# Optimization experiments

Measured on AMD Instinct MI355X. Metric: run time of the kernel, lower is better.

## Reference

```python
import jax, jax.numpy as jnp
import numpy as np

D = 30  # input/hidden size
H1 = 15  # head hidden size


def _rnn_layer(x, Wih, Whh, bih, bhh):
    # x: [B,T,D]; vanilla tanh RNN, h_t = tanh(x_t Wih^T + b_ih + h_{t-1} Whh^T + b_hh)
    xw = jnp.einsum('btd,hd->bth', x, Wih) + bih + bhh  # precompute input projection
    h0 = jnp.zeros((x.shape[0], Whh.shape[0]), x.dtype)

    def step(h, xt):
        h = jnp.tanh(xt + h @ Whh.T)
        return h, h

    _, ys = jax.lax.scan(step, h0, jnp.swapaxes(xw, 0, 1))  # scan over time
    return jnp.swapaxes(ys, 0, 1)  # [B,T,H]


def setup_inputs() -> dict:
    key = jax.random.key(0)
    ks = jax.random.split(key, 16)
    s = 1.0 / np.sqrt(D)
    u = lambda k, shape, sc: jax.random.uniform(k, shape, jnp.float32, -sc, sc)
    return {
        'x': jax.random.normal(ks[0], (4096, 512, D), jnp.float32),
        'Wih1': u(ks[1], (D, D), s), 'Whh1': u(ks[2], (D, D), s),
        'bih1': u(ks[3], (D,), s), 'bhh1': u(ks[4], (D,), s),
        'Wih2': u(ks[5], (D, D), s), 'Whh2': u(ks[6], (D, D), s),
        'bih2': u(ks[7], (D,), s), 'bhh2': u(ks[8], (D,), s),
        'W1': u(ks[9], (H1, D), s), 'b1': u(ks[10], (H1,), s),
        'W2': u(ks[11], (H1, H1), 1.0 / np.sqrt(H1)), 'b2': u(ks[12], (H1,), 1.0 / np.sqrt(H1)),
        'W3': u(ks[13], (1, H1), 1.0 / np.sqrt(H1)), 'b3': u(ks[14], (1,), 1.0 / np.sqrt(H1)),
    }


def reference(x, Wih1, Whh1, bih1, bhh1, Wih2, Whh2, bih2, bhh2, W1, b1, W2, b2, W3, b3):
    out = _rnn_layer(x, Wih1, Whh1, bih1, bhh1)
    # Dropout(0.23) is identity in eval mode
    out = _rnn_layer(out, Wih2, Whh2, bih2, bhh2)
    out = jnp.tanh(out @ W1.T + b1)
    out = jnp.tanh(out @ W2.T + b2)
    return out @ W3.T + b3  # [B,T,1]
```

## Files before the change

### kernel.cpp

```cpp
#include <hip/hip_runtime.h>


namespace {
constexpr int T = 512;
constexpr int D = 30;
constexpr int H = 15;

__device__ __forceinline__ float fast_tanh(float x) {
  float e = __expf(2.0f * x);
  return 1.0f - 2.0f * __builtin_amdgcn_rcpf(e + 1.0f);
}

__device__ __forceinline__ float bcast(float v, int lane) {
  return __int_as_float(__builtin_amdgcn_readlane(__float_as_int(v), lane));
}

__device__ __forceinline__ float lanepull(float v, int byteaddr) {
  return __int_as_float(
      __builtin_amdgcn_ds_bpermute(byteaddr, __float_as_int(v)));
}

#define PIN(v) asm("" : "+v"(v))
}

__global__ __launch_bounds__(256) void xw_precompute(
    const float* __restrict__ x, const float* __restrict__ Wih1,
    const float* __restrict__ bih1, const float* __restrict__ bhh1,
    float* __restrict__ xw) {
  __shared__ float xs[256 * 31];
  const int tid = threadIdx.x;
  const long base = (long)blockIdx.x * (256 * 30);

#pragma unroll
  for (int k = 0; k < 15; ++k) {
    const int idx = k * 512 + tid * 2;
    const float2 v = *(const float2*)(x + base + idx);
    const int row = idx / 30;
    const int col = idx - row * 30;
    xs[row * 31 + col] = v.x;
    xs[row * 31 + col + 1] = v.y;
  }
  __syncthreads();

  float xv[D];
#pragma unroll
  for (int k = 0; k < D; ++k) xv[k] = xs[tid * 31 + k];
#pragma unroll
  for (int i = 0; i < D; ++i) {
    float a = bih1[i] + bhh1[i];
#pragma unroll
    for (int k = 0; k < D; ++k) a = fmaf(Wih1[i * D + k], xv[k], a);
    xs[tid * 31 + i] = a;
  }
  __syncthreads();

#pragma unroll
  for (int k = 0; k < 15; ++k) {
    const int idx = k * 512 + tid * 2;
    const int row = idx / 30;
    const int col = idx - row * 30;
    float2 o;
    o.x = xs[row * 31 + col];
    o.y = xs[row * 31 + col + 1];
    *(float2*)(xw + base + idx) = o;
  }
}

__global__ __attribute__((amdgpu_waves_per_eu(4, 4)))
__launch_bounds__(64) void rnn_head_rec(
    const float* __restrict__ xw,
    const float* __restrict__ Whh1,
    const float* __restrict__ Wih2, const float* __restrict__ Whh2,
    const float* __restrict__ bih2, const float* __restrict__ bhh2,
    const float* __restrict__ W1, const float* __restrict__ b1,
    const float* __restrict__ W2, const float* __restrict__ b2,
    const float* __restrict__ W3, const float* __restrict__ b3,
    float* __restrict__ out) {
  const int j = threadIdx.x;
  const bool lo = (j < 32);
  const int ju = j & 31;
  const int r = (ju < D) ? ju : (D - 1);

  float aw[D], bw[D];
  {
    const float* Ar = (lo ? Whh1 : Wih2) + r * D;
#pragma unroll
    for (int k = 0; k < D; ++k) aw[k] = Ar[k];
#pragma unroll
    for (int k = 0; k < D; ++k) {
      float v;
      if (!lo)
        v = Whh2[r * D + k];
      else if (j < H)
        v = W1[j * D + k];
      else if (j >= 16 && j < 31 && k < H)
        v = W2[(j - 16) * H + k];
      else
        v = 0.0f;
      bw[k] = v;
    }
  }
#pragma unroll
  for (int k = 0; k < D; ++k) {
    PIN(aw[k]);
    PIN(bw[k]);
  }

  int addr2[H];
  {
    const int abase = (j >= 16 && j < 32) ? 0 : 128;
#pragma unroll
    for (int k = 0; k < H; ++k) {
      addr2[k] = abase + 4 * k;
      PIN(addr2[k]);
    }
  }

  float biasA2m = lo ? 0.0f : (bih2[r] + bhh2[r]);
  float biasB = (j < H) ? b1[j] : ((j >= 16 && j < 31) ? b2[j - 16] : 0.0f);
  const bool mid = (j >= 16) && (j < 31);
  float w3v = mid ? W3[j - 16] : 0.0f;
  const float sb3 = b3[0];
  PIN(biasA2m);
  PIN(biasB);
  PIN(w3v);

  const float* xr = xw + (long)blockIdx.x * (T * D);
  float* outp = out + (long)blockIdx.x * T;
  const int cj = r;

  float xvA = xr[cj];
  float xvB = xr[D + cj];

  float rec1 = 0.0f;
  float rec2 = 0.0f;
  float v1p = 0.0f;

  auto step = [&](float& xv, int tpre) -> float {
    const float h1 = fast_tanh(xv + rec1);

    xv = xr[(long)tpre * D + cj];

    float s1[D];
#pragma unroll
    for (int k = 0; k < D; ++k) s1[k] = bcast(h1, k);
    __builtin_amdgcn_sched_barrier(0);
    float p0 = biasA2m, p1 = 0.0f, p2 = 0.0f, p3 = 0.0f;
#pragma unroll
    for (int k = 0; k < D; ++k) {
      if ((k & 3) == 0)
        p0 = fmaf(aw[k], s1[k], p0);
      else if ((k & 3) == 1)
        p1 = fmaf(aw[k], s1[k], p1);
      else if ((k & 3) == 2)
        p2 = fmaf(aw[k], s1[k], p2);
      else
        p3 = fmaf(aw[k], s1[k], p3);
    }
    const float P1 = (p0 + p1) + (p2 + p3);
    rec1 = P1;
    const float h2 = fast_tanh(P1 + rec2);

    const float g = (j < 16) ? v1p : h2;
    float bb[H];
#pragma unroll
    for (int k = 0; k < H; ++k) bb[k] = lanepull(g, addr2[k]);
    float sh[D - H];
#pragma unroll
    for (int k = H; k < D; ++k) sh[k - H] = bcast(h2, 32 + k);
    __builtin_amdgcn_sched_barrier(0);
    float q0 = biasB, q1 = 0.0f, q2 = 0.0f, q3 = 0.0f;
#pragma unroll
    for (int k = 0; k < D; ++k) {
      const float s = (k < H) ? bb[k] : sh[k - H];
      if ((k & 3) == 0)
        q0 = fmaf(bw[k], s, q0);
      else if ((k & 3) == 1)
        q1 = fmaf(bw[k], s, q1);
      else if ((k & 3) == 2)
        q2 = fmaf(bw[k], s, q2);
      else
        q3 = fmaf(bw[k], s, q3);
    }
    const float P2 = (q0 + q1) + (q2 + q3);
    rec2 = P2;
    const float tv = fast_tanh(P2);
    v1p = tv;

    float pv = mid ? (w3v * tv) : 0.0f;
    pv += __shfl_xor(pv, 8, 16);
    pv += __shfl_xor(pv, 4, 16);
    pv += __shfl_xor(pv, 2, 16);
    pv += __shfl_xor(pv, 1, 16);
    return pv;
  };

  float carry = 0.0f;
  for (int t = 0; t < T; t += 2) {
    const float pA = step(xvA, (t + 2 < T) ? (t + 2) : (T - 1));
    if (t > 0 && j == 16) {
      float2 o;
      o.x = carry + sb3;
      o.y = pA + sb3;
      *(float2*)(outp + (t - 2)) = o;
    }
    carry = step(xvB, (t + 3 < T) ? (t + 3) : (T - 1));
  }

  {
    float bb[H];
#pragma unroll
    for (int k = 0; k < H; ++k) bb[k] = lanepull(v1p, addr2[k]);
    float u0 = biasB, u1 = 0.0f, u2 = 0.0f, u3 = 0.0f;
#pragma unroll
    for (int k = 0; k < H; ++k) {
      if ((k & 3) == 0)
        u0 = fmaf(bw[k], bb[k], u0);
      else if ((k & 3) == 1)
        u1 = fmaf(bw[k], bb[k], u1);
      else if ((k & 3) == 2)
        u2 = fmaf(bw[k], bb[k], u2);
      else
        u3 = fmaf(bw[k], bb[k], u3);
    }
    const float v2 = fast_tanh((u0 + u1) + (u2 + u3));
    float pv = mid ? (w3v * v2) : 0.0f;
    pv += __shfl_xor(pv, 8, 16);
    pv += __shfl_xor(pv, 4, 16);
    pv += __shfl_xor(pv, 2, 16);
    pv += __shfl_xor(pv, 1, 16);
    if (j == 16) {
      float2 o;
      o.x = carry + sb3;
      o.y = pv + sb3;
      *(float2*)(outp + (T - 2)) = o;
    }
  }
}

__global__ __launch_bounds__(64, 3) void rnn_head_fused_fb(
    const float* __restrict__ x,
    const float* __restrict__ Wih1, const float* __restrict__ Whh1,
    const float* __restrict__ bih1, const float* __restrict__ bhh1,
    const float* __restrict__ Wih2, const float* __restrict__ Whh2,
    const float* __restrict__ bih2, const float* __restrict__ bhh2,
    const float* __restrict__ W1, const float* __restrict__ b1,
    const float* __restrict__ W2, const float* __restrict__ b2,
    const float* __restrict__ W3, const float* __restrict__ b3,
    float* __restrict__ out) {
  const int j = threadIdx.x;
  const bool lo = (j < 32);
  const int ju = j & 31;
  const int r = (ju < D) ? ju : (D - 1);

  float dk[D], aw[D], bw[D];
  {
    const float* Dr = Wih1 + r * D;
    const float* Ar = (lo ? Whh1 : Wih2) + r * D;
#pragma unroll
    for (int k = 0; k < D; ++k) {
      dk[k] = Dr[k];
      aw[k] = Ar[k];
    }
#pragma unroll
    for (int k = 0; k < D; ++k) {
      float v;
      if (!lo)
        v = Whh2[r * D + k];
      else if (j < H)
        v = W1[j * D + k];
      else if (j >= 16 && j < 31 && k < H)
        v = W2[(j - 16) * H + k];
      else
        v = 0.0f;
      bw[k] = v;
    }
  }
#pragma unroll
  for (int k = 0; k < D; ++k) {
    PIN(dk[k]);
    PIN(aw[k]);
    PIN(bw[k]);
  }

  float biasA = lo ? (bih1[r] + bhh1[r]) : (bih2[r] + bhh2[r]);
  float biasB = (j < H) ? b1[j] : ((j >= 16 && j < 31) ? b2[j - 16] : 0.0f);
  const bool mid = (j >= 16) && (j < 31);
  float w3v = mid ? W3[j - 16] : 0.0f;
  const float sb3 = b3[0];
  PIN(biasA);
  PIN(biasB);
  PIN(w3v);

  const float* xr = x + (long)blockIdx.x * (T * D);
  float* outp = out + (long)blockIdx.x * T;
  const int cj = r;

  float xvA = xr[cj];
  float xvB = xr[D + cj];
  float rec1 = 0.0f, rec2 = 0.0f;

  auto step = [&](float& xv, int tpre) -> float {
    float a0 = biasA, a1 = rec1, a2 = 0.0f, a3 = 0.0f;
#pragma unroll
    for (int k = 0; k < D; ++k) {
      const float s = bcast(xv, k);
      if ((k & 3) == 0)
        a0 = fmaf(dk[k], s, a0);
      else if ((k & 3) == 1)
        a1 = fmaf(dk[k], s, a1);
      else if ((k & 3) == 2)
        a2 = fmaf(dk[k], s, a2);
      else
        a3 = fmaf(dk[k], s, a3);
    }
    const float h1 = fast_tanh((a0 + a1) + (a2 + a3));
    xv = xr[(long)tpre * D + cj];

    float p0 = 0.0f, p1 = 0.0f, p2 = 0.0f, p3 = 0.0f;
#pragma unroll
    for (int k = 0; k < D; ++k) {
      const float s = bcast(h1, k);
      if ((k & 3) == 0)
        p0 = fmaf(aw[k], s, p0);
      else if ((k & 3) == 1)
        p1 = fmaf(aw[k], s, p1);
      else if ((k & 3) == 2)
        p2 = fmaf(aw[k], s, p2);
      else
        p3 = fmaf(aw[k], s, p3);
    }
    const float P1 = (p0 + p1) + (p2 + p3);
    rec1 = P1;
    const float h2 = fast_tanh(P1 + biasA + rec2);

    float q0 = biasB, q1 = 0.0f, q2 = 0.0f, q3 = 0.0f;
#pragma unroll
    for (int k = 0; k < D; ++k) {
      const float s = bcast(h2, 32 + k);
      if ((k & 3) == 0)
        q0 = fmaf(bw[k], s, q0);
      else if ((k & 3) == 1)
        q1 = fmaf(bw[k], s, q1);
      else if ((k & 3) == 2)
        q2 = fmaf(bw[k], s, q2);
      else
        q3 = fmaf(bw[k], s, q3);
    }
    const float P2 = (q0 + q1) + (q2 + q3);
    rec2 = P2;
    const float v1 = fast_tanh(P2);

    float u0 = biasB, u1 = 0.0f, u2 = 0.0f, u3 = 0.0f;
#pragma unroll
    for (int k = 0; k < H; ++k) {
      const float s = bcast(v1, k);
      if ((k & 3) == 0)
        u0 = fmaf(bw[k], s, u0);
      else if ((k & 3) == 1)
        u1 = fmaf(bw[k], s, u1);
      else if ((k & 3) == 2)
        u2 = fmaf(bw[k], s, u2);
      else
        u3 = fmaf(bw[k], s, u3);
    }
    const float v2 = fast_tanh((u0 + u1) + (u2 + u3));

    float pv = mid ? (w3v * v2) : 0.0f;
    pv += __shfl_xor(pv, 8, 16);
    pv += __shfl_xor(pv, 4, 16);
    pv += __shfl_xor(pv, 2, 16);
    pv += __shfl_xor(pv, 1, 16);
    return pv;
  };

  for (int t = 0; t < T; t += 2) {
    const float pA = step(xvA, (t + 2 < T) ? (t + 2) : (T - 1));
    const float pB = step(xvB, (t + 3 < T) ? (t + 3) : (T - 1));
    if (j == 16) {
      float2 o;
      o.x = pA + sb3;
      o.y = pB + sb3;
      *(float2*)(outp + t) = o;
    }
  }
}

extern "C" void kernel_launch(void* const* d_in, const int* in_sizes, int n_in,
                              void* d_out, int out_size, void* d_ws,
                              size_t ws_size, hipStream_t stream) {
  const float* x = (const float*)d_in[0];
  const float* Wih1 = (const float*)d_in[1];
  const float* Whh1 = (const float*)d_in[2];
  const float* bih1 = (const float*)d_in[3];
  const float* bhh1 = (const float*)d_in[4];
  const float* Wih2 = (const float*)d_in[5];
  const float* Whh2 = (const float*)d_in[6];
  const float* bih2 = (const float*)d_in[7];
  const float* bhh2 = (const float*)d_in[8];
  const float* W1 = (const float*)d_in[9];
  const float* b1 = (const float*)d_in[10];
  const float* W2 = (const float*)d_in[11];
  const float* b2 = (const float*)d_in[12];
  const float* W3 = (const float*)d_in[13];
  const float* b3 = (const float*)d_in[14];

  const int B = in_sizes[0] / (T * D);
  const size_t xw_bytes = (size_t)B * T * D * sizeof(float);

  if (ws_size >= xw_bytes) {
    float* xw = (float*)d_ws;
    const long rows = (long)B * T;
    hipLaunchKernelGGL(xw_precompute, dim3(rows / 256), dim3(256), 0, stream,
                       x, Wih1, bih1, bhh1, xw);
    hipLaunchKernelGGL(rnn_head_rec, dim3(B), dim3(64), 0, stream, xw, Whh1,
                       Wih2, Whh2, bih2, bhh2, W1, b1, W2, b2, W3, b3,
                       (float*)d_out);
  } else {
    hipLaunchKernelGGL(rnn_head_fused_fb, dim3(B), dim3(64), 0, stream, x,
                       Wih1, Whh1, bih1, bhh1, Wih2, Whh2, bih2, bhh2, W1, b1,
                       W2, b2, W3, b3, (float*)d_out);
  }
}
```

Before: 953.1 us.

## Fuse input projection into recurrent kernel via per-pass LDS staging

Removes the separate xw_precompute kernel and its global workspace round-trip. The recurrent kernel now loads 64 timesteps of x into shared memory, computes the Wih1 projection for them in place, and then runs the recurrence from LDS. This cuts a full write and read of the projected activations to HBM. In exchange it adds barriers and a serial projection phase inside each block, which stalls the latency-bound recurrence between passes.

```diff
diff --git a/kernel.cpp b/kernel.cpp
--- a/kernel.cpp
+++ b/kernel.cpp
@@ -5,6 +5,8 @@
 constexpr int T = 512;
 constexpr int D = 30;
 constexpr int H = 15;
+constexpr int PASS = 64;
+constexpr int NPASS = T / PASS;
 
 __device__ __forceinline__ float fast_tanh(float x) {
   float e = __expf(2.0f * x);
@@ -23,59 +25,18 @@
 #define PIN(v) asm("" : "+v"(v))
 }
 
-__global__ __launch_bounds__(256) void xw_precompute(
-    const float* __restrict__ x, const float* __restrict__ Wih1,
+__global__ __attribute__((amdgpu_waves_per_eu(4, 4)))
+__launch_bounds__(64) void rnn_fused2(
+    const float* __restrict__ x,
+    const float* __restrict__ Wih1, const float* __restrict__ Whh1,
     const float* __restrict__ bih1, const float* __restrict__ bhh1,
-    float* __restrict__ xw) {
-  __shared__ float xs[256 * 31];
-  const int tid = threadIdx.x;
-  const long base = (long)blockIdx.x * (256 * 30);
-
-#pragma unroll
-  for (int k = 0; k < 15; ++k) {
-    const int idx = k * 512 + tid * 2;
-    const float2 v = *(const float2*)(x + base + idx);
-    const int row = idx / 30;
-    const int col = idx - row * 30;
-    xs[row * 31 + col] = v.x;
-    xs[row * 31 + col + 1] = v.y;
-  }
-  __syncthreads();
-
-  float xv[D];
-#pragma unroll
-  for (int k = 0; k < D; ++k) xv[k] = xs[tid * 31 + k];
-#pragma unroll
-  for (int i = 0; i < D; ++i) {
-    float a = bih1[i] + bhh1[i];
-#pragma unroll
-    for (int k = 0; k < D; ++k) a = fmaf(Wih1[i * D + k], xv[k], a);
-    xs[tid * 31 + i] = a;
-  }
-  __syncthreads();
-
-#pragma unroll
-  for (int k = 0; k < 15; ++k) {
-    const int idx = k * 512 + tid * 2;
-    const int row = idx / 30;
-    const int col = idx - row * 30;
-    float2 o;
-    o.x = xs[row * 31 + col];
-    o.y = xs[row * 31 + col + 1];
-    *(float2*)(xw + base + idx) = o;
-  }
-}
-
-__global__ __attribute__((amdgpu_waves_per_eu(4, 4)))
-__launch_bounds__(64) void rnn_head_rec(
-    const float* __restrict__ xw,
-    const float* __restrict__ Whh1,
     const float* __restrict__ Wih2, const float* __restrict__ Whh2,
     const float* __restrict__ bih2, const float* __restrict__ bhh2,
     const float* __restrict__ W1, const float* __restrict__ b1,
     const float* __restrict__ W2, const float* __restrict__ b2,
     const float* __restrict__ W3, const float* __restrict__ b3,
     float* __restrict__ out) {
+  __shared__ float xs[PASS * 31];
   const int j = threadIdx.x;
   const bool lo = (j < 32);
   const int ju = j & 31;
@@ -118,28 +79,22 @@
 
   float biasA2m = lo ? 0.0f : (bih2[r] + bhh2[r]);
   float biasB = (j < H) ? b1[j] : ((j >= 16 && j < 31) ? b2[j - 16] : 0.0f);
-  const bool mid = (j >= 16) && (j < 31);
-  float w3v = mid ? W3[j - 16] : 0.0f;
+  float w3v = (j >= 16 && j < 31) ? W3[j - 16] : 0.0f;
   const float sb3 = b3[0];
   PIN(biasA2m);
   PIN(biasB);
   PIN(w3v);
 
-  const float* xr = xw + (long)blockIdx.x * (T * D);
+  const float* xrow = x + (long)blockIdx.x * (T * D);
   float* outp = out + (long)blockIdx.x * T;
   const int cj = r;
-
-  float xvA = xr[cj];
-  float xvB = xr[D + cj];
 
   float rec1 = 0.0f;
   float rec2 = 0.0f;
   float v1p = 0.0f;
 
-  auto step = [&](float& xv, int tpre) -> float {
+  auto step = [&](float xv) -> float {
     const float h1 = fast_tanh(xv + rec1);
-
-    xv = xr[(long)tpre * D + cj];
 
     float s1[D];
 #pragma unroll
@@ -187,7 +142,7 @@
     const float tv = fast_tanh(P2);
     v1p = tv;
 
-    float pv = mid ? (w3v * tv) : 0.0f;
+    float pv = w3v * tv;
     pv += __shfl_xor(pv, 8, 16);
     pv += __shfl_xor(pv, 4, 16);
     pv += __shfl_xor(pv, 2, 16);
@@ -196,15 +151,50 @@
   };
 
   float carry = 0.0f;
-  for (int t = 0; t < T; t += 2) {
-    const float pA = step(xvA, (t + 2 < T) ? (t + 2) : (T - 1));
-    if (t > 0 && j == 16) {
-      float2 o;
-      o.x = carry + sb3;
-      o.y = pA + sb3;
-      *(float2*)(outp + (t - 2)) = o;
-    }
-    carry = step(xvB, (t + 3 < T) ? (t + 3) : (T - 1));
+#pragma unroll 1
+  for (int p = 0; p < NPASS; ++p) {
+    const float* src = xrow + p * (PASS * D);
+#pragma unroll
+    for (int it = 0; it < 15; ++it) {
+      const int idx = it * 128 + j * 2;
+      const float2 v = *(const float2*)(src + idx);
+      const int row = idx / 30;
+      const int col = idx - row * 30;
+      xs[row * 31 + col] = v.x;
+      xs[row * 31 + col + 1] = v.y;
+    }
+    __syncthreads();
+
+    {
+      float xv[D];
+#pragma unroll
+      for (int k = 0; k < D; ++k) xv[k] = xs[j * 31 + k];
+      __syncthreads();
+#pragma unroll
+      for (int i = 0; i < D; ++i) {
+        float a = bih1[i] + bhh1[i];
+#pragma unroll
+        for (int k = 0; k < D; ++k) a = fmaf(Wih1[i * D + k], xv[k], a);
+        xs[j * 31 + i] = a;
+      }
+    }
+    __syncthreads();
+
+#pragma unroll 1
+    for (int tl = 0; tl < PASS; tl += 2) {
+      const int t = p * PASS + tl;
+      const float xvA = xs[tl * 31 + cj];
+      const float xvB = xs[(tl + 1) * 31 + cj];
+      const float pA = step(xvA);
+      if ((p | tl) && j == 16) {
+        float2 o;
+        o.x = carry + sb3;
+        o.y = pA + sb3;
+        *(float2*)(outp + (t - 2)) = o;
+      }
+      carry = step(xvB);
+    }
+    __syncthreads();
   }
 
   {
@@ -224,7 +214,7 @@
         u3 = fmaf(bw[k], bb[k], u3);
     }
     const float v2 = fast_tanh((u0 + u1) + (u2 + u3));
-    float pv = mid ? (w3v * v2) : 0.0f;
+    float pv = w3v * v2;
     pv += __shfl_xor(pv, 8, 16);
     pv += __shfl_xor(pv, 4, 16);
     pv += __shfl_xor(pv, 2, 16);
@@ -234,154 +224,6 @@
       o.x = carry + sb3;
       o.y = pv + sb3;
       *(float2*)(outp + (T - 2)) = o;
-    }
-  }
-}
-
-__global__ __launch_bounds__(64, 3) void rnn_head_fused_fb(
-    const float* __restrict__ x,
-    const float* __restrict__ Wih1, const float* __restrict__ Whh1,
-    const float* __restrict__ bih1, const float* __restrict__ bhh1,
-    const float* __restrict__ Wih2, const float* __restrict__ Whh2,
-    const float* __restrict__ bih2, const float* __restrict__ bhh2,
-    const float* __restrict__ W1, const float* __restrict__ b1,
-    const float* __restrict__ W2, const float* __restrict__ b2,
-    const float* __restrict__ W3, const float* __restrict__ b3,
-    float* __restrict__ out) {
-  const int j = threadIdx.x;
-  const bool lo = (j < 32);
-  const int ju = j & 31;
-  const int r = (ju < D) ? ju : (D - 1);
-
-  float dk[D], aw[D], bw[D];
-  {
-    const float* Dr = Wih1 + r * D;
-    const float* Ar = (lo ? Whh1 : Wih2) + r * D;
-#pragma unroll
-    for (int k = 0; k < D; ++k) {
-      dk[k] = Dr[k];
-      aw[k] = Ar[k];
-    }
-#pragma unroll
-    for (int k = 0; k < D; ++k) {
-      float v;
-      if (!lo)
-        v = Whh2[r * D + k];
-      else if (j < H)
-        v = W1[j * D + k];
-      else if (j >= 16 && j < 31 && k < H)
-        v = W2[(j - 16) * H + k];
-      else
-        v = 0.0f;
-      bw[k] = v;
-    }
-  }
-#pragma unroll
-  for (int k = 0; k < D; ++k) {
-    PIN(dk[k]);
-    PIN(aw[k]);
-    PIN(bw[k]);
-  }
-
-  float biasA = lo ? (bih1[r] + bhh1[r]) : (bih2[r] + bhh2[r]);
-  float biasB = (j < H) ? b1[j] : ((j >= 16 && j < 31) ? b2[j - 16] : 0.0f);
-  const bool mid = (j >= 16) && (j < 31);
-  float w3v = mid ? W3[j - 16] : 0.0f;
-  const float sb3 = b3[0];
-  PIN(biasA);
-  PIN(biasB);
-  PIN(w3v);
-
-  const float* xr = x + (long)blockIdx.x * (T * D);
-  float* outp = out + (long)blockIdx.x * T;
-  const int cj = r;
-
-  float xvA = xr[cj];
-  float xvB = xr[D + cj];
-  float rec1 = 0.0f, rec2 = 0.0f;
-
-  auto step = [&](float& xv, int tpre) -> float {
-    float a0 = biasA, a1 = rec1, a2 = 0.0f, a3 = 0.0f;
-#pragma unroll
-    for (int k = 0; k < D; ++k) {
-      const float s = bcast(xv, k);
-      if ((k & 3) == 0)
-        a0 = fmaf(dk[k], s, a0);
-      else if ((k & 3) == 1)
-        a1 = fmaf(dk[k], s, a1);
-      else if ((k & 3) == 2)
-        a2 = fmaf(dk[k], s, a2);
-      else
-        a3 = fmaf(dk[k], s, a3);
-    }
-    const float h1 = fast_tanh((a0 + a1) + (a2 + a3));
-    xv = xr[(long)tpre * D + cj];
-
-    float p0 = 0.0f, p1 = 0.0f, p2 = 0.0f, p3 = 0.0f;
-#pragma unroll
-    for (int k = 0; k < D; ++k) {
-      const float s = bcast(h1, k);
-      if ((k & 3) == 0)
-        p0 = fmaf(aw[k], s, p0);
-      else if ((k & 3) == 1)
-        p1 = fmaf(aw[k], s, p1);
-      else if ((k & 3) == 2)
-        p2 = fmaf(aw[k], s, p2);
-      else
-        p3 = fmaf(aw[k], s, p3);
-    }
-    const float P1 = (p0 + p1) + (p2 + p3);
-    rec1 = P1;
-    const float h2 = fast_tanh(P1 + biasA + rec2);
-
-    float q0 = biasB, q1 = 0.0f, q2 = 0.0f, q3 = 0.0f;
-#pragma unroll
-    for (int k = 0; k < D; ++k) {
-      const float s = bcast(h2, 32 + k);
-      if ((k & 3) == 0)
-        q0 = fmaf(bw[k], s, q0);
-      else if ((k & 3) == 1)
-        q1 = fmaf(bw[k], s, q1);
-      else if ((k & 3) == 2)
-        q2 = fmaf(bw[k], s, q2);
-      else
-        q3 = fmaf(bw[k], s, q3);
-    }
-    const float P2 = (q0 + q1) + (q2 + q3);
-    rec2 = P2;
-    const float v1 = fast_tanh(P2);
-
-    float u0 = biasB, u1 = 0.0f, u2 = 0.0f, u3 = 0.0f;
-#pragma unroll
-    for (int k = 0; k < H; ++k) {
-      const float s = bcast(v1, k);
-      if ((k & 3) == 0)
-        u0 = fmaf(bw[k], s, u0);
-      else if ((k & 3) == 1)
-        u1 = fmaf(bw[k], s, u1);
-      else if ((k & 3) == 2)
-        u2 = fmaf(bw[k], s, u2);
-      else
-        u3 = fmaf(bw[k], s, u3);
-    }
-    const float v2 = fast_tanh((u0 + u1) + (u2 + u3));
-
-    float pv = mid ? (w3v * v2) : 0.0f;
-    pv += __shfl_xor(pv, 8, 16);
-    pv += __shfl_xor(pv, 4, 16);
-    pv += __shfl_xor(pv, 2, 16);
-    pv += __shfl_xor(pv, 1, 16);
-    return pv;
-  };
-
-  for (int t = 0; t < T; t += 2) {
-    const float pA = step(xvA, (t + 2 < T) ? (t + 2) : (T - 1));
-    const float pB = step(xvB, (t + 3 < T) ? (t + 3) : (T - 1));
-    if (j == 16) {
-      float2 o;
-      o.x = pA + sb3;
-      o.y = pB + sb3;
-      *(float2*)(outp + t) = o;
     }
   }
 }
@@ -406,19 +248,10 @@
   const float* b3 = (const float*)d_in[14];
 
   const int B = in_sizes[0] / (T * D);
-  const size_t xw_bytes = (size_t)B * T * D * sizeof(float);
-
-  if (ws_size >= xw_bytes) {
-    float* xw = (float*)d_ws;
-    const long rows = (long)B * T;
-    hipLaunchKernelGGL(xw_precompute, dim3(rows / 256), dim3(256), 0, stream,
-                       x, Wih1, bih1, bhh1, xw);
-    hipLaunchKernelGGL(rnn_head_rec, dim3(B), dim3(64), 0, stream, xw, Whh1,
-                       Wih2, Whh2, bih2, bhh2, W1, b1, W2, b2, W3, b3,
-                       (float*)d_out);
-  } else {
-    hipLaunchKernelGGL(rnn_head_fused_fb, dim3(B), dim3(64), 0, stream, x,
-                       Wih1, Whh1, bih1, bhh1, Wih2, Whh2, bih2, bhh2, W1, b1,
-                       W2, b2, W3, b3, (float*)d_out);
-  }
-}
+  (void)d_ws;
+  (void)ws_size;
+
+  hipLaunchKernelGGL(rnn_fused2, dim3(B), dim3(64), 0, stream, x, Wih1, Whh1,
+                     bih1, bhh1, Wih2, Whh2, bih2, bhh2, W1, b1, W2, b2, W3,
+                     b3, (float*)d_out);
+}
```

Result: slower. 985.0 us (+3.3%).
